# Kernel optimization log

Hardware: AMD Instinct MI355X
Metric: run time of the kernel (lower is better)

Reference implementation:

```python
import jax, jax.numpy as jnp
import numpy as np

B, LT, LI, D, H, K = 32, 512, 576, 768, 8, 512


def setup_inputs() -> dict:
    key = jax.random.key(0)
    ks = jax.random.split(key, 10)
    s = 0.02
    return {
        "text_hidden_states": jax.random.normal(ks[0], (B, LT, D), jnp.float32),
        "image_hidden_states": jax.random.normal(ks[1], (B, LI, D), jnp.float32),
        "text_mask": jnp.ones((B, LT), jnp.int32),
        "Wb": jax.random.normal(ks[2], (H, D, D), jnp.float32) * s,   # per-head Linear weights [out,in]
        "Wv": jax.random.normal(ks[3], (K, D), jnp.float32) * s,
        "Wq": jax.random.normal(ks[4], (K, D), jnp.float32) * s,
        "Whv": jax.random.normal(ks[5], (K,), jnp.float32) * s,
        "Whq": jax.random.normal(ks[6], (K,), jnp.float32) * s,
        "Wo": jax.random.normal(ks[7], (D, D * H), jnp.float32) * s,  # output_proj weight [out,in]
        "bo": jnp.zeros((D,), jnp.float32),
    }


def reference(text_hidden_states, image_hidden_states, text_mask, Wb, Wv, Wq, Whv, Whq, Wo, bo):
    text, image = text_hidden_states, image_hidden_states
    # per-head text projection (torch Linear: x @ W.T), batched over heads
    pt = jnp.einsum('bxe,hfe->hbxf', text, Wb)                 # [H,B,LT,D]
    aff = jnp.einsum('hbxe,bye->hbxy', pt, image)              # [H,B,LT,LI]
    wv_v = jnp.einsum('bye,ke->byk', image, Wv)                # [B,LI,K] (head-shared)
    wq_q = jnp.einsum('bxe,ke->bxk', text, Wq)                 # [B,LT,K]
    wqqc = jnp.einsum('bxk,hbxy->hbyk', wq_q, aff)             # [H,B,LI,K]
    wvvc = jnp.einsum('byk,hbxy->hbxk', wv_v, aff)             # [H,B,LT,K]
    h_v = jnp.tanh(wv_v[None] + wqqc)
    h_q = jnp.tanh(wq_q[None] + wvvc)
    att_v = jax.nn.softmax(jnp.einsum('hbyk,k->hby', h_v, Whv), axis=-1)  # over image tokens
    att_q = jax.nn.softmax(jnp.einsum('hbxk,k->hbx', h_q, Whq), axis=-1)  # over text tokens
    ctx_v = jnp.einsum('hby,byd->hbd', att_v, image)
    ctx_q = jnp.einsum('hbx,bxd->hbd', att_q, text)
    head_out = ctx_v + ctx_q                                   # [H,B,D]
    combined = jnp.transpose(head_out, (1, 0, 2)).reshape(text.shape[0], -1)  # [B,H*D]
    return combined @ Wo.T + bo
```

## Files before the change

### kernel.cpp

```cpp
#include <hip/hip_runtime.h>
#include <math.h>

#define B_  32
#define LT_ 512
#define LI_ 576
#define LIP 640
#define D_  768
#define H_  8
#define K_  512
#define NTOK  (LI_ + LT_)
#define CSPLIT 8
#define TPB   (NTOK / CSPLIT)
#define NHEAD ((long)H_ * B_ * D_)

typedef __attribute__((ext_vector_type(4))) short short4v;
typedef __attribute__((ext_vector_type(8))) unsigned short ushort8;
typedef __attribute__((ext_vector_type(8))) _Float16 f16x8;
typedef __attribute__((ext_vector_type(4))) float f32x4;

__device__ __forceinline__ unsigned short f2h(float x) {
  _Float16 h = (_Float16)x;
  return __builtin_bit_cast(unsigned short, h);
}
__device__ __forceinline__ float h2f(unsigned short u) {
  return (float)__builtin_bit_cast(_Float16, u);
}
__device__ __forceinline__ float ftanh(float x) {
  float e = __expf(2.f * x);
  return 1.f - 2.f * __builtin_amdgcn_rcpf(e + 1.f);
}

__device__ __forceinline__ void gl_lds16(const void* g, void* l) {
  __builtin_amdgcn_global_load_lds(
      (const __attribute__((address_space(1))) void*)g,
      (__attribute__((address_space(3))) void*)l, 16, 0, 0);
}

__device__ __forceinline__ f16x8 lds_read16(const unsigned short* p) {
  f16x8 r;
  const __attribute__((address_space(3))) unsigned short* lp =
      (const __attribute__((address_space(3))) unsigned short*)p;
  asm volatile("ds_read_b128 %0, %1" : "=v"(r) : "v"(lp));
  return r;
}

#define EPI_PLAIN 0
#define EPI_T     1
#define EPI_TANH  2
#define EPI_OUT   3

struct Seg {
  const unsigned short *A, *B;
  unsigned short *C, *CT;
  const unsigned short* base;
  const float* wvec;
  float* outv;
  long sA, sB, sC, sCT, sBase;
  int Kd, lda, ldb;
  int gx, gy, nblk, epi, Mlim, valid, ldc, ldt;
};
struct Params { Seg s0, s1, s2; };

__global__ __launch_bounds__(256, 3) void mfma_seg(Params p)
{
  const int orig = blockIdx.x, nwg = gridDim.x;
  const int q8 = nwg >> 3, r8 = nwg & 7;
  const int xcd = orig & 7, idx = orig >> 3;
  const int wg = (xcd < r8 ? xcd * (q8 + 1) : r8 * (q8 + 1) + (xcd - r8) * q8) + idx;

  Seg sg; int local;
  if (wg < p.s0.nblk)                      { sg = p.s0; local = wg; }
  else if (wg < p.s0.nblk + p.s1.nblk)     { sg = p.s1; local = wg - p.s0.nblk; }
  else                                     { sg = p.s2; local = wg - p.s0.nblk - p.s1.nblk; }

  const int bx = local % sg.gx;
  const int tmp2 = local / sg.gx;
  const int by = tmp2 % sg.gy, bz = tmp2 / sg.gy;

  __shared__ unsigned short LDSU[24576];

  const int t = threadIdx.x, lane = t & 63, w = t >> 6;
  const int wr = w >> 1, wc = w & 1;
  const int m0 = bx * 128, n0 = by * 128;
  const int Kd = sg.Kd, lda = sg.lda, ldb = sg.ldb, ldc = sg.ldc;
  const unsigned short* A  = sg.A + (long)bz * sg.sA;
  const unsigned short* Bm = sg.B + (long)bz * sg.sB;

  const int srow = w * 16 + (lane >> 2);
  const int cswz = ((lane & 3) ^ ((srow >> 1) & 3)) * 8;
  const bool clampA = (m0 + 128 > sg.Mlim);
  const unsigned short* aSrc = A  + (long)(m0 + srow) * lda + cswz;
  const unsigned short* bSrc = Bm + (long)(n0 + srow) * ldb + cswz;
  const int ldsLane = w * 512 + lane * 8;

  f32x4 acc[4][4];
  #pragma unroll
  for (int i = 0; i < 4; ++i)
    #pragma unroll
    for (int j = 0; j < 4; ++j)
      acc[i][j] = (f32x4){0.f, 0.f, 0.f, 0.f};

  const int rl = lane & 15, g = lane >> 4;
  const int aslot = (g ^ ((rl >> 1) & 3)) << 3;

  auto stage = [&](int bufi, int k0) {
    unsigned short* Ab = LDSU + bufi * 8192;
    unsigned short* Bb = Ab + 4096;
    if (!clampA) {
      gl_lds16(aSrc + k0,                 Ab + ldsLane);
      gl_lds16(aSrc + (long)64 * lda + k0, Ab + ldsLane + 2048);
    } else {
      int r0 = m0 + srow, r1 = r0 + 64;
      if (r0 >= sg.Mlim) r0 = sg.Mlim - 1;
      if (r1 >= sg.Mlim) r1 = sg.Mlim - 1;
      gl_lds16(A + (long)r0 * lda + cswz + k0, Ab + ldsLane);
      gl_lds16(A + (long)r1 * lda + cswz + k0, Ab + ldsLane + 2048);
    }
    gl_lds16(bSrc + k0,                 Bb + ldsLane);
    gl_lds16(bSrc + (long)64 * ldb + k0, Bb + ldsLane + 2048);
  };

  const int nt = Kd >> 5;
  stage(0, 0);
  if (nt > 1) stage(1, 32);
  if (nt > 2) stage(2, 64);
  int cur = 0;
  for (int tt = 0; tt < nt; ++tt) {
    const int ahead = nt - 1 - tt;
    if (ahead >= 2)      asm volatile("s_waitcnt vmcnt(8)" ::: "memory");
    else if (ahead == 1) asm volatile("s_waitcnt vmcnt(4)" ::: "memory");
    else                 asm volatile("s_waitcnt vmcnt(0)" ::: "memory");
    __builtin_amdgcn_s_barrier();

    const unsigned short* Ab = LDSU + cur * 8192;
    const unsigned short* Bb = Ab + 4096;
    f16x8 af[4], bf[4];
    #pragma unroll
    for (int i = 0; i < 4; ++i)
      af[i] = lds_read16(&Ab[(wr * 64 + i * 16 + rl) * 32 + aslot]);
    #pragma unroll
    for (int j = 0; j < 4; ++j)
      bf[j] = lds_read16(&Bb[(wc * 64 + j * 16 + rl) * 32 + aslot]);
    asm volatile("s_waitcnt lgkmcnt(0)" ::: "memory");
    __builtin_amdgcn_sched_barrier(0);

    __builtin_amdgcn_s_setprio(1);
    #pragma unroll
    for (int i = 0; i < 4; ++i)
      #pragma unroll
      for (int j = 0; j < 4; ++j)
        acc[i][j] = __builtin_amdgcn_mfma_f32_16x16x32_f16(af[i], bf[j], acc[i][j], 0, 0, 0);
    __builtin_amdgcn_s_setprio(0);

    __builtin_amdgcn_s_barrier();
    if (tt + 3 < nt) stage(cur, (tt + 3) << 5);
    cur = (cur == 2) ? 0 : cur + 1;
  }

  const int rg = lane >> 4;
  if (sg.epi <= EPI_T) {
    unsigned short* C = sg.C + (long)bz * sg.sC;
    unsigned short hv[4][4][4];
    #pragma unroll
    for (int i = 0; i < 4; ++i)
      #pragma unroll
      for (int j = 0; j < 4; ++j)
        #pragma unroll
        for (int rr = 0; rr < 4; ++rr) {
          int ml = wr * 64 + i * 16 + rg * 4 + rr;
          int nl = wc * 64 + j * 16 + rl;
          hv[i][j][rr] = f2h(acc[i][j][rr]);
          if (m0 + ml < sg.Mlim)
            C[(long)(m0 + ml) * ldc + n0 + nl] = hv[i][j][rr];
        }
    if (sg.epi == EPI_T) {
      unsigned short* CT = sg.CT + (long)bz * sg.sCT;
      #pragma unroll
      for (int i = 0; i < 4; ++i)
        #pragma unroll
        for (int j = 0; j < 4; ++j) {
          int nl = wc * 64 + j * 16 + rl;
          int mh = wr * 64 + i * 16 + rg * 4;
          *(short4v*)&LDSU[nl * 136 + mh] = (short4v){
              (short)hv[i][j][0], (short)hv[i][j][1],
              (short)hv[i][j][2], (short)hv[i][j][3]};
        }
      __syncthreads();
      #pragma unroll
      for (int rr = 0; rr < 8; ++rr) {
        int rn = rr * 16 + (t >> 4);
        int m8 = (t & 15) * 8;
        if (m0 + m8 < sg.Mlim)
          *(ushort8*)(CT + (long)(n0 + rn) * sg.ldt + m0 + m8) =
              *(const ushort8*)&LDSU[rn * 136 + m8];
      }
    }
  } else if (sg.epi == EPI_TANH) {
    const unsigned short* base = sg.base + (long)bz * sg.sBase;
    float* outp = sg.outv + (long)bz * sg.valid;
    #pragma unroll
    for (int i = 0; i < 4; ++i)
      #pragma unroll
      for (int rr = 0; rr < 4; ++rr) {
        int row = m0 + wr * 64 + i * 16 + rg * 4 + rr;
        if (row < sg.Mlim) {
          float s = 0.f;
          #pragma unroll
          for (int j = 0; j < 4; ++j) {
            int col = n0 + wc * 64 + j * 16 + rl;
            float v = acc[i][j][rr] + h2f(base[(long)row * ldc + col]);
            s += ftanh(v) * sg.wvec[col];
          }
          s += __shfl_xor(s, 1, 64);
          s += __shfl_xor(s, 2, 64);
          s += __shfl_xor(s, 4, 64);
          s += __shfl_xor(s, 8, 64);
          if (rl == 0 && row < sg.valid)
            atomicAdd(&outp[row], s);
        }
      }
  } else {
    float* outp = sg.outv;
    if (wr == 0) {
      #pragma unroll
      for (int i = 0; i < 2; ++i)
        #pragma unroll
        for (int rr = 0; rr < 4; ++rr) {
          int row = i * 16 + rg * 4 + rr;
          #pragma unroll
          for (int j = 0; j < 4; ++j) {
            int col = n0 + wc * 64 + j * 16 + rl;
            atomicAdd(&outp[(long)row * ldc + col], acc[i][j][rr]);
          }
        }
    }
  }
}

struct CSeg { const float* src; unsigned short* dst; long n8; };

__global__ __launch_bounds__(256) void cast_multi(
    CSeg c0, CSeg c1, CSeg c2, CSeg c3, CSeg c4)
{
  long i = (long)blockIdx.x * 256 + threadIdx.x;
  const float* src; unsigned short* dst;
  if      (i < c0.n8)                 { src = c0.src; dst = c0.dst; }
  else if ((i -= c0.n8) < c1.n8)      { src = c1.src; dst = c1.dst; }
  else if ((i -= c1.n8) < c2.n8)      { src = c2.src; dst = c2.dst; }
  else if ((i -= c2.n8) < c3.n8)      { src = c3.src; dst = c3.dst; }
  else if ((i -= c3.n8) < c4.n8)      { src = c4.src; dst = c4.dst; }
  else return;
  float4 v0 = ((const float4*)src)[i * 2];
  float4 v1 = ((const float4*)src)[i * 2 + 1];
  ushort8 o;
  o[0] = f2h(v0.x); o[1] = f2h(v0.y); o[2] = f2h(v0.z); o[3] = f2h(v0.w);
  o[4] = f2h(v1.x); o[5] = f2h(v1.y); o[6] = f2h(v1.z); o[7] = f2h(v1.w);
  *(ushort8*)(dst + i * 8) = o;
}

__global__ __launch_bounds__(256) void cast_pad_image(
    const float* __restrict__ in, unsigned short* __restrict__ out)
{
  long tid = (long)blockIdx.x * 256 + threadIdx.x;
  const long tot = (long)B_ * LIP * (D_ / 8);
  if (tid >= tot) return;
  int e8 = (int)(tid % (D_ / 8));
  long rw = tid / (D_ / 8);
  int y  = (int)(rw % LIP);
  long b = rw / LIP;
  ushort8 o;
  if (y < LI_) {
    const float* p = in + ((b * LI_ + y) * D_ + e8 * 8);
    float4 v0 = *(const float4*)p, v1 = *(const float4*)(p + 4);
    o[0] = f2h(v0.x); o[1] = f2h(v0.y); o[2] = f2h(v0.z); o[3] = f2h(v0.w);
    o[4] = f2h(v1.x); o[5] = f2h(v1.y); o[6] = f2h(v1.z); o[7] = f2h(v1.w);
  } else {
    #pragma unroll
    for (int j = 0; j < 8; ++j) o[j] = 0;
  }
  *(ushort8*)(out + rw * D_ + e8 * 8) = o;
}

__global__ __launch_bounds__(256) void zero_f32(float* __restrict__ p, long n) {
  long i = (long)blockIdx.x * 256 + threadIdx.x;
  if (i < n) p[i] = 0.f;
}

__global__ __launch_bounds__(256) void init_out(
    const float* __restrict__ bo, float* __restrict__ out)
{
  int i = blockIdx.x * 256 + threadIdx.x;
  out[i] = bo[i % D_];
}

__global__ __launch_bounds__(256) void softmax_att(
    const float* __restrict__ lv, const float* __restrict__ lq,
    float* __restrict__ attvG, float* __restrict__ attqG)
{
  const int b = blockIdx.x, h = blockIdx.y;
  const int t = threadIdx.x;
  __shared__ float buf[LI_];
  __shared__ float red[4];

  const float* lvp = lv + ((long)h * B_ + b) * LI_;
  float m = -1e30f;
  for (int i = t; i < LI_; i += 256) m = fmaxf(m, lvp[i]);
  #pragma unroll
  for (int o = 32; o > 0; o >>= 1) m = fmaxf(m, __shfl_down(m, o, 64));
  if ((t & 63) == 0) red[t >> 6] = m;
  __syncthreads();
  m = fmaxf(fmaxf(red[0], red[1]), fmaxf(red[2], red[3]));
  __syncthreads();
  float s = 0.f;
  for (int i = t; i < LI_; i += 256) { float e = __expf(lvp[i] - m); buf[i] = e; s += e; }
  #pragma unroll
  for (int o = 32; o > 0; o >>= 1) s += __shfl_down(s, o, 64);
  if ((t & 63) == 0) red[t >> 6] = s;
  __syncthreads();
  s = red[0] + red[1] + red[2] + red[3];
  {
    float inv = 1.f / s;
    float* op = attvG + ((long)h * B_ + b) * LI_;
    for (int i = t; i < LI_; i += 256) op[i] = buf[i] * inv;
  }
  __syncthreads();

  const float* lqp = lq + ((long)h * B_ + b) * LT_;
  m = -1e30f;
  for (int i = t; i < LT_; i += 256) m = fmaxf(m, lqp[i]);
  #pragma unroll
  for (int o = 32; o > 0; o >>= 1) m = fmaxf(m, __shfl_down(m, o, 64));
  if ((t & 63) == 0) red[t >> 6] = m;
  __syncthreads();
  m = fmaxf(fmaxf(red[0], red[1]), fmaxf(red[2], red[3]));
  __syncthreads();
  s = 0.f;
  for (int i = t; i < LT_; i += 256) { float e = __expf(lqp[i] - m); buf[i] = e; s += e; }
  #pragma unroll
  for (int o = 32; o > 0; o >>= 1) s += __shfl_down(s, o, 64);
  if ((t & 63) == 0) red[t >> 6] = s;
  __syncthreads();
  s = red[0] + red[1] + red[2] + red[3];
  {
    float inv = 1.f / s;
    float* op = attqG + ((long)h * B_ + b) * LT_;
    for (int i = t; i < LT_; i += 256) op[i] = buf[i] * inv;
  }
}

__global__ __launch_bounds__(256) void ctx_part(
    const float* __restrict__ attvG, const float* __restrict__ attqG,
    const unsigned short* __restrict__ text_h,
    float* __restrict__ head_part)
{
  const int b = blockIdx.x, d0 = blockIdx.y * 128, s = blockIdx.z;
  const int t = threadIdx.x, dl = t & 127, g = t >> 7;
  const long IMG_OFF = (long)B_ * LT_ * D_;
  __shared__ float wts[H_][TPB];
  __shared__ long  roff[TPB];
  __shared__ float red[H_][128];
  const int tok0 = s * TPB;
  for (int i = t; i < H_ * TPB; i += 256) {
    int h = i / TPB, j = i % TPB, tok = tok0 + j;
    wts[h][j] = tok < LI_ ? attvG[((long)h * B_ + b) * LI_ + tok]
                          : attqG[((long)h * B_ + b) * LT_ + (tok - LI_)];
  }
  if (t < TPB) {
    int tok = tok0 + t;
    roff[t] = tok < LI_ ? IMG_OFF + ((long)b * LIP + tok) * D_
                        : ((long)b * LT_ + (tok - LI_)) * D_;
  }
  __syncthreads();
  float acc[H_];
  #pragma unroll
  for (int h = 0; h < H_; ++h) acc[h] = 0.f;
  #pragma unroll 4
  for (int j = g; j < TPB; j += 2) {
    float val = h2f(text_h[roff[j] + d0 + dl]);
    #pragma unroll
    for (int h = 0; h < H_; ++h) acc[h] = fmaf(wts[h][j], val, acc[h]);
  }
  if (g == 1) {
    #pragma unroll
    for (int h = 0; h < H_; ++h) red[h][dl] = acc[h];
  }
  __syncthreads();
  if (g == 0) {
    float* hp = head_part + (long)s * NHEAD;
    #pragma unroll
    for (int h = 0; h < H_; ++h)
      hp[((long)h * B_ + b) * D_ + d0 + dl] = acc[h] + red[h][dl];
  }
}

__global__ __launch_bounds__(256) void reduce_head(
    const float* __restrict__ head_part, unsigned short* __restrict__ head16)
{
  long i = (long)blockIdx.x * 256 + threadIdx.x;
  float s = 0.f;
  #pragma unroll
  for (int p = 0; p < CSPLIT; ++p) s += head_part[(long)p * NHEAD + i];
  int d = (int)(i % D_);
  long hb = i / D_;
  int b = (int)(hb % B_), h = (int)(hb / B_);
  head16[(long)b * (H_ * D_) + (long)h * D_ + d] = f2h(s);
}

extern "C" void kernel_launch(void* const* d_in, const int* in_sizes, int n_in,
                              void* d_out, int out_size, void* d_ws, size_t ws_size,
                              hipStream_t stream)
{
  const float* text  = (const float*)d_in[0];
  const float* image = (const float*)d_in[1];
  const float* Wb  = (const float*)d_in[3];
  const float* Wv  = (const float*)d_in[4];
  const float* Wq  = (const float*)d_in[5];
  const float* Whv = (const float*)d_in[6];
  const float* Whq = (const float*)d_in[7];
  const float* Wo  = (const float*)d_in[8];
  const float* bo  = (const float*)d_in[9];
  float* out = (float*)d_out;

  const long N_TEXT = (long)B_ * LT_ * D_;
  const long N_IMGP = (long)B_ * LIP * D_;
  const long N_WV   = (long)K_ * D_;
  const long N_WB   = (long)H_ * D_ * D_;
  const long N_WO   = (long)D_ * H_ * D_;
  const long N_WVV  = (long)B_ * LIP * K_;
  const long N_WQQ  = (long)B_ * LT_ * K_;
  const long N_PT   = (long)B_ * LT_ * D_;
  const long N_AFF  = (long)B_ * LT_ * LIP;
  const long N_LV   = (long)H_ * B_ * LI_;
  const long N_LQ   = (long)H_ * B_ * LT_;
  const long N_H16  = (long)B_ * H_ * D_;

  unsigned short* wsu = (unsigned short*)d_ws;
  long off = 0;
  unsigned short* text_h  = wsu + off; off += N_TEXT;
  unsigned short* image_p = wsu + off; off += N_IMGP;
  unsigned short* Wv_h    = wsu + off; off += N_WV;
  unsigned short* Wq_h    = wsu + off; off += N_WV;
  unsigned short* Wb_h    = wsu + off; off += N_WB;
  unsigned short* Wo_h    = wsu + off; off += N_WO;
  unsigned short* wv_v    = wsu + off; off += N_WVV;
  unsigned short* wq_q    = wsu + off; off += N_WQQ;
  unsigned short* wv_vT   = wsu + off; off += N_WVV;
  unsigned short* wq_qT   = wsu + off; off += N_WQQ;
  unsigned short* pt_h    = wsu + off; off += N_PT;
  unsigned short* aff     = wsu + off; off += N_AFF;
  unsigned short* affT    = wsu + off; off += N_AFF;
  unsigned short* head16  = wsu + off; off += N_H16;
  float* lv        = (float*)(wsu + off);
  float* lq        = lv + N_LV;
  float* attvG     = lq + N_LQ;
  float* attqG     = attvG + N_LV;
  float* head_part = attqG + N_LQ;
  const size_t need = (size_t)off * 2 +
      (size_t)(2 * (N_LV + N_LQ) + CSPLIT * NHEAD) * 4;
  if (ws_size < need) return;

  dim3 blk(256);

  {
    CSeg c0{text, text_h, N_TEXT / 8};
    CSeg c1{Wv,   Wv_h,   N_WV / 8};
    CSeg c2{Wq,   Wq_h,   N_WV / 8};
    CSeg c3{Wb,   Wb_h,   N_WB / 8};
    CSeg c4{Wo,   Wo_h,   N_WO / 8};
    long tot8 = c0.n8 + c1.n8 + c2.n8 + c3.n8 + c4.n8;
    cast_multi<<<(unsigned)((tot8 + 255) / 256), blk, 0, stream>>>(c0, c1, c2, c3, c4);
  }
  cast_pad_image<<<(unsigned)((B_ * LIP * (D_ / 8) + 255) / 256), blk, 0, stream>>>(image, image_p);
  zero_f32<<<(unsigned)((N_LV + N_LQ + 255) / 256), blk, 0, stream>>>(lv, N_LV + N_LQ);
  init_out<<<(unsigned)(B_ * D_ / 256), blk, 0, stream>>>(bo, out);

  Seg zs{};  zs.nblk = 0;

  {
    Seg s0{}; s0.A = image_p; s0.B = Wv_h; s0.C = wv_v; s0.CT = wv_vT;
    s0.sA = (long)LIP * D_; s0.sC = (long)LIP * K_; s0.sCT = (long)K_ * LIP;
    s0.Kd = D_; s0.lda = D_; s0.ldb = D_;
    s0.gx = 5; s0.gy = 4; s0.nblk = 5 * 4 * B_; s0.epi = EPI_T;
    s0.Mlim = LIP; s0.ldc = K_; s0.ldt = LIP;

    Seg s1{}; s1.A = text_h; s1.B = Wq_h; s1.C = wq_q; s1.CT = wq_qT;
    s1.sA = (long)LT_ * D_; s1.sC = (long)LT_ * K_; s1.sCT = (long)K_ * LT_;
    s1.Kd = D_; s1.lda = D_; s1.ldb = D_;
    s1.gx = 4; s1.gy = 4; s1.nblk = 4 * 4 * B_; s1.epi = EPI_T;
    s1.Mlim = LT_; s1.ldc = K_; s1.ldt = LT_;

    Seg s2{}; s2.A = text_h; s2.B = Wb_h; s2.C = pt_h;
    s2.Kd = D_; s2.lda = D_; s2.ldb = D_;
    s2.gx = 128; s2.gy = 6; s2.nblk = 128 * 6; s2.epi = EPI_PLAIN;
    s2.Mlim = B_ * LT_; s2.ldc = D_;

    Params P{s0, s1, s2};
    mfma_seg<<<s0.nblk + s1.nblk + s2.nblk, blk, 0, stream>>>(P);
  }

  for (int h = 0; h < H_; ++h) {
    {
      Seg s0{}; s0.A = pt_h; s0.B = image_p; s0.C = aff; s0.CT = affT;
      s0.sA = (long)LT_ * D_; s0.sB = (long)LIP * D_;
      s0.sC = (long)LT_ * LIP; s0.sCT = (long)LIP * LT_;
      s0.Kd = D_; s0.lda = D_; s0.ldb = D_;
      s0.gx = 4; s0.gy = 5; s0.nblk = 4 * 5 * B_; s0.epi = EPI_T;
      s0.Mlim = LT_; s0.ldc = LIP; s0.ldt = LT_;
      Params P{s0, zs, zs};
      mfma_seg<<<s0.nblk, blk, 0, stream>>>(P);
    }
    {
      Seg s0{}; s0.A = affT; s0.B = wq_qT;
      s0.base = wv_v; s0.wvec = Whv; s0.outv = lv + (long)h * B_ * LI_;
      s0.sA = (long)LIP * LT_; s0.sB = (long)K_ * LT_; s0.sBase = (long)LIP * K_;
      s0.Kd = LT_; s0.lda = LT_; s0.ldb = LT_;
      s0.gx = 5; s0.gy = 4; s0.nblk = 5 * 4 * B_; s0.epi = EPI_TANH;
      s0.Mlim = LIP; s0.valid = LI_; s0.ldc = K_;

      Seg s1{}; s1.A = aff; s1.B = wv_vT;
      s1.base = wq_q; s1.wvec = Whq; s1.outv = lq + (long)h * B_ * LT_;
      s1.sA = (long)LT_ * LIP; s1.sB = (long)K_ * LIP; s1.sBase = (long)LT_ * K_;
      s1.Kd = LIP; s1.lda = LIP; s1.ldb = LIP;
      s1.gx = 4; s1.gy = 4; s1.nblk = 4 * 4 * B_; s1.epi = EPI_TANH;
      s1.Mlim = LT_; s1.valid = LT_; s1.ldc = K_;

      Seg s2 = zs;
      if (h < H_ - 1) {
        s2.A = text_h; s2.B = Wb_h + (long)(h + 1) * D_ * D_; s2.C = pt_h;
        s2.Kd = D_; s2.lda = D_; s2.ldb = D_;
        s2.gx = 128; s2.gy = 6; s2.nblk = 128 * 6; s2.epi = EPI_PLAIN;
        s2.Mlim = B_ * LT_; s2.ldc = D_;
      }
      Params P{s0, s1, s2};
      mfma_seg<<<s0.nblk + s1.nblk + s2.nblk, blk, 0, stream>>>(P);
    }
  }

  softmax_att<<<dim3(B_, H_), blk, 0, stream>>>(lv, lq, attvG, attqG);
  ctx_part<<<dim3(B_, D_ / 128, CSPLIT), blk, 0, stream>>>(attvG, attqG, text_h, head_part);
  reduce_head<<<(unsigned)(NHEAD / 256), blk, 0, stream>>>(head_part, head16);

  {
    Seg s0{}; s0.A = head16; s0.B = Wo_h; s0.outv = out;
    s0.sA = (long)(H_ * D_ / 8); s0.sB = (long)(H_ * D_ / 8);
    s0.Kd = H_ * D_ / 8; s0.lda = H_ * D_; s0.ldb = H_ * D_;
    s0.gx = 1; s0.gy = 6; s0.nblk = 1 * 6 * 8; s0.epi = EPI_OUT;
    s0.Mlim = B_; s0.valid = B_; s0.ldc = D_;
    Params P{s0, zs, zs};
    mfma_seg<<<s0.nblk, blk, 0, stream>>>(P);
  }
}
```

Before: 972.2 us.

## Double-buffer LDS fragment registers to overlap LDS reads with MFMA

Restructures the GEMM main loop into a two-step unrolled pipeline. Fragments for the next K-tile are read from LDS into a second register set while MFMAs run on the current set. Global-to-LDS staging is issued before each MFMA batch, with adjusted vmcnt/lgkmcnt waits and barriers. The goal is to hide LDS read latency behind matrix math, at the cost of doubled fragment registers (possible occupancy loss) and more intricate synchronization; an extra __syncthreads is added before the transpose epilogue reuses LDS.

```diff
diff --git a/kernel.cpp b/kernel.cpp
--- a/kernel.cpp
+++ b/kernel.cpp
@@ -120,30 +120,18 @@
     gl_lds16(bSrc + (long)64 * ldb + k0, Bb + ldsLane + 2048);
   };
 
-  const int nt = Kd >> 5;
-  stage(0, 0);
-  if (nt > 1) stage(1, 32);
-  if (nt > 2) stage(2, 64);
-  int cur = 0;
-  for (int tt = 0; tt < nt; ++tt) {
-    const int ahead = nt - 1 - tt;
-    if (ahead >= 2)      asm volatile("s_waitcnt vmcnt(8)" ::: "memory");
-    else if (ahead == 1) asm volatile("s_waitcnt vmcnt(4)" ::: "memory");
-    else                 asm volatile("s_waitcnt vmcnt(0)" ::: "memory");
-    __builtin_amdgcn_s_barrier();
-
-    const unsigned short* Ab = LDSU + cur * 8192;
+  f16x8 af0[4], bf0[4], af1[4], bf1[4];
+  auto ldfrags = [&](int bufi, f16x8* af, f16x8* bf) {
+    const unsigned short* Ab = LDSU + bufi * 8192;
     const unsigned short* Bb = Ab + 4096;
-    f16x8 af[4], bf[4];
     #pragma unroll
     for (int i = 0; i < 4; ++i)
       af[i] = lds_read16(&Ab[(wr * 64 + i * 16 + rl) * 32 + aslot]);
     #pragma unroll
     for (int j = 0; j < 4; ++j)
       bf[j] = lds_read16(&Bb[(wc * 64 + j * 16 + rl) * 32 + aslot]);
-    asm volatile("s_waitcnt lgkmcnt(0)" ::: "memory");
-    __builtin_amdgcn_sched_barrier(0);
-
+  };
+  auto mma = [&](const f16x8* af, const f16x8* bf) {
     __builtin_amdgcn_s_setprio(1);
     #pragma unroll
     for (int i = 0; i < 4; ++i)
@@ -151,10 +139,44 @@
       for (int j = 0; j < 4; ++j)
         acc[i][j] = __builtin_amdgcn_mfma_f32_16x16x32_f16(af[i], bf[j], acc[i][j], 0, 0, 0);
     __builtin_amdgcn_s_setprio(0);
-
+  };
+
+  const int nt = Kd >> 5;
+  stage(0, 0); stage(1, 32); stage(2, 64);
+  asm volatile("s_waitcnt vmcnt(8)" ::: "memory");
+  __builtin_amdgcn_s_barrier();
+  ldfrags(0, af0, bf0);
+  asm volatile("s_waitcnt vmcnt(4)" ::: "memory");
+  __builtin_amdgcn_s_barrier();
+
+  for (int tt = 0; tt < nt; tt += 2) {
+    if (tt + 1 < nt) {
+      ldfrags((tt + 1) % 3, af1, bf1);
+      asm volatile("s_waitcnt lgkmcnt(8)" ::: "memory");
+    } else {
+      asm volatile("s_waitcnt lgkmcnt(0)" ::: "memory");
+    }
+    __builtin_amdgcn_sched_barrier(0);
     __builtin_amdgcn_s_barrier();
-    if (tt + 3 < nt) stage(cur, (tt + 3) << 5);
-    cur = (cur == 2) ? 0 : cur + 1;
+    if (tt + 3 < nt) stage(tt % 3, (tt + 3) << 5);
+    mma(af0, bf0);
+    if (tt + 3 < nt)      asm volatile("s_waitcnt vmcnt(4)" ::: "memory");
+    else if (tt + 2 < nt) asm volatile("s_waitcnt vmcnt(0)" ::: "memory");
+    if (tt + 2 < nt) __builtin_amdgcn_s_barrier();
+
+    if (tt + 2 < nt) {
+      ldfrags((tt + 2) % 3, af0, bf0);
+      asm volatile("s_waitcnt lgkmcnt(8)" ::: "memory");
+    } else {
+      asm volatile("s_waitcnt lgkmcnt(0)" ::: "memory");
+    }
+    __builtin_amdgcn_sched_barrier(0);
+    __builtin_amdgcn_s_barrier();
+    if (tt + 4 < nt) stage((tt + 1) % 3, (tt + 4) << 5);
+    mma(af1, bf1);
+    if (tt + 4 < nt)      asm volatile("s_waitcnt vmcnt(4)" ::: "memory");
+    else if (tt + 3 < nt) asm volatile("s_waitcnt vmcnt(0)" ::: "memory");
+    if (tt + 3 < nt) __builtin_amdgcn_s_barrier();
   }
 
   const int rg = lane >> 4;
@@ -175,6 +197,7 @@
         }
     if (sg.epi == EPI_T) {
       unsigned short* CT = sg.CT + (long)bz * sg.sCT;
+      __syncthreads();
       #pragma unroll
       for (int i = 0; i < 4; ++i)
         #pragma unroll
```

Measured after the change: 990.7 us. Within noise of the previous version (+1.9%).
